# Optimization experiments

Hardware: AMD Instinct MI355X
Metric: run time of the kernel (lower is better)

## Reference

```python
import jax, jax.numpy as jnp
import numpy as np

B, S, D, H = 2, 2048, 2048, 16
HD = D // H
SCALE = 1.0 / np.sqrt(HD)


def setup_inputs() -> dict:
    key = jax.random.key(0)
    ks = jax.random.split(key, 11)
    xav = np.sqrt(6.0 / (D + D))  # xavier uniform bound for square weights
    def w(k):
        return jax.random.uniform(k, (D, D), jnp.float32, -xav, xav)
    return {
        "query": jax.random.normal(ks[0], (B, S, D), jnp.float32),
        "key": jax.random.normal(ks[1], (B, S, D), jnp.float32),
        "value": jax.random.normal(ks[2], (B, S, D), jnp.float32),
        "Wq": w(ks[3]), "bq": jnp.zeros((D,), jnp.float32),
        "Wk": w(ks[4]), "bk": jnp.zeros((D,), jnp.float32),
        "Wv": w(ks[5]), "bv": jnp.zeros((D,), jnp.float32),
        "Wo": w(ks[6]), "bo": jnp.zeros((D,), jnp.float32),
    }


def reference(query, key, value, Wq, bq, Wk, bk, Wv, bv, Wo, bo):
    # projections (torch Linear: x @ W.T + b)
    q = query @ Wq.T + bq
    k = key @ Wk.T + bk
    v = value @ Wv.T + bv
    # [B, H, S, HD]
    q = q.reshape(B, S, H, HD).transpose(0, 2, 1, 3)
    k = k.reshape(B, S, H, HD).transpose(0, 2, 1, 3)
    v = v.reshape(B, S, H, HD).transpose(0, 2, 1, 3)
    scores = jnp.einsum("bhqd,bhkd->bhqk", q, k) * SCALE
    causal = jnp.triu(jnp.ones((S, S), bool), k=1)
    scores = jnp.where(causal, -jnp.inf, scores)
    attn = jax.nn.softmax(scores, axis=-1)  # dropout p=0.0 -> identity
    out = jnp.einsum("bhqk,bhkd->bhqd", attn, v)
    out = out.transpose(0, 2, 1, 3).reshape(B, S, D)
    return out @ Wo.T + bo
```

## Files before the change

### kernel.cpp

```cpp
#include <hip/hip_runtime.h>
#include <hip/hip_bf16.h>


#define LOG2E 1.44269504088896340736f

typedef __attribute__((ext_vector_type(8))) short short8;
typedef __attribute__((ext_vector_type(4))) short short4b;
typedef __attribute__((ext_vector_type(4))) float floatx4;

__device__ __forceinline__ short f2bf(float f) {
  unsigned int u = __builtin_bit_cast(unsigned int, f);
  u += 0x7FFFu + ((u >> 16) & 1u);
  return (short)(u >> 16);
}

__device__ __forceinline__ short4b pack4bf(float a, float b, float c, float d) {
  __hip_bfloat162 lo = __float22bfloat162_rn(float2{a, b});
  __hip_bfloat162 hi = __float22bfloat162_rn(float2{c, d});
  short4b r;
  r[0] = __builtin_bit_cast(short, lo.x); r[1] = __builtin_bit_cast(short, lo.y);
  r[2] = __builtin_bit_cast(short, hi.x); r[3] = __builtin_bit_cast(short, hi.y);
  return r;
}

__device__ __forceinline__ void gl_lds16(const void* g, void* l) {
  __builtin_amdgcn_global_load_lds(
      (const __attribute__((address_space(1))) unsigned int*)g,
      (__attribute__((address_space(3))) unsigned int*)l, 16, 0, 0);
}

__global__ __launch_bounds__(256) void cvt7_k(
    const float* __restrict__ s0, const float* __restrict__ s1,
    const float* __restrict__ s2, const float* __restrict__ s3,
    const float* __restrict__ s4, const float* __restrict__ s5,
    const float* __restrict__ s6,
    unsigned short* __restrict__ d0, unsigned short* __restrict__ d1,
    unsigned short* __restrict__ d2, unsigned short* __restrict__ d3,
    unsigned short* __restrict__ d4, unsigned short* __restrict__ d5,
    unsigned short* __restrict__ d6, int nAct, int nW)
{
  const float* s; unsigned short* d; int n, iters;
  switch (blockIdx.y) {
    case 0: s = s0; d = d0; n = nAct; iters = 4; break;
    case 1: s = s1; d = d1; n = nAct; iters = 4; break;
    case 2: s = s2; d = d2; n = nAct; iters = 4; break;
    case 3: s = s3; d = d3; n = nW;   iters = 1; break;
    case 4: s = s4; d = d4; n = nW;   iters = 1; break;
    case 5: s = s5; d = d5; n = nW;   iters = 1; break;
    default: s = s6; d = d6; n = nW;  iters = 1; break;
  }
#pragma unroll 1
  for (int c = 0; c < iters; ++c) {
    const long i = ((long)(blockIdx.x + c * 2048) * 256 + threadIdx.x) * 8;
    if (i < n) {
      float4 a = *(const float4*)(s + i);
      float4 b = *(const float4*)(s + i + 4);
      short8 v = (short8){f2bf(a.x), f2bf(a.y), f2bf(a.z), f2bf(a.w),
                          f2bf(b.x), f2bf(b.y), f2bf(b.z), f2bf(b.w)};
      *(short8*)(d + i) = v;
    }
  }
}

template<bool OUT_BF16, bool VT_OUT>
__global__ __launch_bounds__(512, 1) void gemm8_k(
    const unsigned short* __restrict__ A, const unsigned short* __restrict__ Bt,
    const float* __restrict__ bias, void* __restrict__ Cptr,
    int M, int N, int K, float alpha)
{
  __shared__ __align__(16) unsigned short As[3][256 * 64];
  __shared__ __align__(16) unsigned short Bs[3][128 * 64];
  (void)M;

  const int tid  = threadIdx.x;
  const int lane = tid & 63;
  const int wave = tid >> 6;
  const int quad = lane >> 4;
  const int l16  = lane & 15;
  const int lx7  = l16 & 7;
  const int wm   = wave >> 1, wn = wave & 1;

  int bx, by;
  if (gridDim.x == 16 && gridDim.y == 16) {
    const int lin  = (int)(blockIdx.y * 16 + blockIdx.x);
    const int xcd  = lin & 7;
    const int slot = lin >> 3;
    bx = (xcd & 1) * 8 + (slot & 7);
    by = (xcd >> 1) * 4 + (slot >> 3);
  } else { bx = (int)blockIdx.x; by = (int)blockIdx.y; }
  const long bm  = (long)by * 256;
  const long bn  = (long)bx * 128;

  const unsigned short* gA[4]; int lAo[4];
  const unsigned short* gB[2]; int lBo[2];
#pragma unroll
  for (int j = 0; j < 4; ++j) {
    const int pa = ((j >> 1) * 16 + wave * 2 + (j & 1)) * 64 + lane;
    const int r = pa >> 3, cp = pa & 7, cs = cp ^ (r & 7);
    gA[j]  = A + (bm + r) * (long)K + cs * 8;
    lAo[j] = pa * 8;
  }
#pragma unroll
  for (int j = 0; j < 2; ++j) {
    const int pb = (wave * 2 + j) * 64 + lane;
    const int r = pb >> 3, cp = pb & 7, cs = cp ^ (r & 7);
    gB[j]  = Bt + (bn + r) * (long)K + cs * 8;
    lBo[j] = pb * 8;
  }

  floatx4 acc[4][4];
#pragma unroll
  for (int i = 0; i < 4; ++i)
#pragma unroll
    for (int j = 0; j < 4; ++j) acc[i][j] = (floatx4){0.f, 0.f, 0.f, 0.f};

  const int NT = K >> 6;

#pragma unroll
  for (int j = 0; j < 4; ++j) gl_lds16(gA[j], &As[0][lAo[j]]);
#pragma unroll
  for (int j = 0; j < 2; ++j) gl_lds16(gB[j], &Bs[0][lBo[j]]);
  if (NT > 1) {
#pragma unroll
    for (int j = 0; j < 4; ++j) gl_lds16(gA[j] + 64, &As[1][lAo[j]]);
#pragma unroll
    for (int j = 0; j < 2; ++j) gl_lds16(gB[j] + 64, &Bs[1][lBo[j]]);
    asm volatile("s_waitcnt vmcnt(6)" ::: "memory");
  } else {
    asm volatile("s_waitcnt vmcnt(0)" ::: "memory");
  }
  __builtin_amdgcn_s_barrier();

  int cur3 = 0;
  for (int t = 0; t < NT; ++t) {
    int nx2 = cur3 + 2; if (nx2 >= 3) nx2 -= 3;
    const long kk2 = (long)(t + 2) * 64;
    const bool st2 = (t + 2) < NT;
    const bool st1 = (t + 1) < NT;
    const unsigned short* Ab = As[cur3];
    const unsigned short* Bb = Bs[cur3];

    if (st2) {
      gl_lds16(gA[0] + kk2, &As[nx2][lAo[0]]);
      gl_lds16(gA[1] + kk2, &As[nx2][lAo[1]]);
      gl_lds16(gA[2] + kk2, &As[nx2][lAo[2]]);
      gl_lds16(gA[3] + kk2, &As[nx2][lAo[3]]);
      gl_lds16(gB[0] + kk2, &Bs[nx2][lBo[0]]);
      gl_lds16(gB[1] + kk2, &Bs[nx2][lBo[1]]);
    }

    short8 af[4][2], bf[4][2];
#pragma unroll
    for (int mt = 0; mt < 4; ++mt)
#pragma unroll
      for (int ks = 0; ks < 2; ++ks)
        af[mt][ks] = *(const short8*)&Ab[(wm * 64 + mt * 16 + l16) * 64 +
                                         (((ks * 4 + quad) ^ lx7) * 8)];
#pragma unroll
    for (int nt = 0; nt < 4; ++nt)
#pragma unroll
      for (int ks = 0; ks < 2; ++ks)
        bf[nt][ks] = *(const short8*)&Bb[(wn * 64 + nt * 16 + l16) * 64 +
                                         (((ks * 4 + quad) ^ lx7) * 8)];

    __builtin_amdgcn_s_setprio(1);
#pragma unroll
    for (int nt = 0; nt < 4; ++nt)
#pragma unroll
      for (int mt = 0; mt < 4; ++mt) {
        acc[mt][nt] = __builtin_amdgcn_mfma_f32_16x16x32_bf16(af[mt][0], bf[nt][0], acc[mt][nt], 0, 0, 0);
        acc[mt][nt] = __builtin_amdgcn_mfma_f32_16x16x32_bf16(af[mt][1], bf[nt][1], acc[mt][nt], 0, 0, 0);
      }
    __builtin_amdgcn_s_setprio(0);

    if (st1) {
      if (st2) asm volatile("s_waitcnt vmcnt(6)" ::: "memory");
      else     asm volatile("s_waitcnt vmcnt(0)" ::: "memory");
    }
    __builtin_amdgcn_s_barrier();

    cur3 = cur3 + 1 >= 3 ? 0 : cur3 + 1;
  }

  if (VT_OUT) {
    __syncthreads();
    unsigned short* Ct = &As[0][0];
#pragma unroll
    for (int nt = 0; nt < 4; ++nt) {
      const int col_l = wn * 64 + nt * 16 + l16;
      const float bval = bias[bn + col_l];
#pragma unroll
      for (int mt = 0; mt < 4; ++mt) {
        const int row_l = wm * 64 + mt * 16 + quad * 4;
#pragma unroll
        for (int rg = 0; rg < 4; ++rg)
          Ct[col_l * 264 + row_l + rg] = (unsigned short)f2bf((acc[mt][nt][rg] + bval) * alpha);
      }
    }
    __syncthreads();
    const int b  = (int)(bm >> 11);
    const int s0 = (int)(bm & 2047);
    const int d   = tid >> 2;
    const int seg = tid & 3;
    unsigned short* dst = (unsigned short*)Cptr +
        ((long)(b * 16 + bx) * 128 + d) * 2048 + s0 + seg * 64;
    const unsigned short* src = &Ct[d * 264 + seg * 64];
#pragma unroll
    for (int c = 0; c < 8; ++c)
      *(uint4*)(dst + c * 8) = *(const uint4*)(src + c * 8);
  } else {
#pragma unroll
    for (int nt = 0; nt < 4; ++nt) {
      const long col = bn + wn * 64 + nt * 16 + l16;
      const float bval = bias[col];
#pragma unroll
      for (int mt = 0; mt < 4; ++mt) {
#pragma unroll
        for (int rg = 0; rg < 4; ++rg) {
          const long row = bm + wm * 64 + mt * 16 + quad * 4 + rg;
          const float v = (acc[mt][nt][rg] + bval) * alpha;
          if (OUT_BF16) ((unsigned short*)Cptr)[row * (long)N + col] = (unsigned short)f2bf(v);
          else          ((float*)Cptr)[row * (long)N + col] = v;
        }
      }
    }
  }
}

template<bool A_BF16, bool OUT_BF16, bool VT_OUT>
__global__ __launch_bounds__(256, 2) void gemm_bias_k(
    const void* __restrict__ Aptr, const float* __restrict__ Bt,
    const float* __restrict__ bias, void* __restrict__ Cptr,
    int M, int N, int K, float alpha)
{
  __shared__ __align__(16) unsigned short smem[128 * 136];
  unsigned short* As = smem;
  unsigned short* Bs = smem + 128 * 40;

  const int tid  = threadIdx.x;
  const int lane = tid & 63;
  const int wave = tid >> 6;
  const int quad = lane >> 4;
  const int l16  = lane & 15;
  const int wr   = wave >> 1, wc = wave & 1;
  const long bm  = (long)blockIdx.y * 128;
  const long bn  = (long)blockIdx.x * 128;

  floatx4 acc[4][4];
#pragma unroll
  for (int i = 0; i < 4; ++i)
#pragma unroll
    for (int j = 0; j < 4; ++j) acc[i][j] = (floatx4){0.f, 0.f, 0.f, 0.f};

  const int srow = tid >> 2;
  const int cc   = tid & 3;

  for (int k0 = 0; k0 < K; k0 += 32) {
    __syncthreads();
#pragma unroll
    for (int r = 0; r < 2; ++r) {
      const int row = srow + r * 64;
      short8 av, bv;
      if (A_BF16) {
        av = *(const short8*)((const unsigned short*)Aptr + (bm + row) * (long)K + k0 + cc * 8);
      } else {
        const float* ap = (const float*)Aptr + (bm + row) * (long)K + k0 + cc * 8;
        float4 f0 = *(const float4*)ap;
        float4 f1 = *(const float4*)(ap + 4);
        av = (short8){f2bf(f0.x), f2bf(f0.y), f2bf(f0.z), f2bf(f0.w),
                      f2bf(f1.x), f2bf(f1.y), f2bf(f1.z), f2bf(f1.w)};
      }
      {
        const float* bp = Bt + (bn + row) * (long)K + k0 + cc * 8;
        float4 g0 = *(const float4*)bp;
        float4 g1 = *(const float4*)(bp + 4);
        bv = (short8){f2bf(g0.x), f2bf(g0.y), f2bf(g0.z), f2bf(g0.w),
                      f2bf(g1.x), f2bf(g1.y), f2bf(g1.z), f2bf(g1.w)};
      }
      *(short8*)&As[row * 40 + cc * 8] = av;
      *(short8*)&Bs[row * 40 + cc * 8] = bv;
    }
    __syncthreads();

    short8 af[4], bf[4];
#pragma unroll
    for (int t = 0; t < 4; ++t) {
      af[t] = *(const short8*)&As[(wr * 64 + t * 16 + l16) * 40 + quad * 8];
      bf[t] = *(const short8*)&Bs[(wc * 64 + t * 16 + l16) * 40 + quad * 8];
    }
#pragma unroll
    for (int mt = 0; mt < 4; ++mt)
#pragma unroll
      for (int nt = 0; nt < 4; ++nt)
        acc[mt][nt] = __builtin_amdgcn_mfma_f32_16x16x32_bf16(af[mt], bf[nt], acc[mt][nt], 0, 0, 0);
  }

  if (VT_OUT) {
    __syncthreads();
    unsigned short* Ct = smem;
#pragma unroll
    for (int nt = 0; nt < 4; ++nt) {
      const long col = bn + wc * 64 + nt * 16 + l16;
      const float bval = bias[col];
      const int col_l = wc * 64 + nt * 16 + l16;
#pragma unroll
      for (int mt = 0; mt < 4; ++mt) {
        const int row_l = wr * 64 + mt * 16 + quad * 4;
#pragma unroll
        for (int rg = 0; rg < 4; ++rg)
          Ct[col_l * 136 + row_l + rg] = (unsigned short)f2bf((acc[mt][nt][rg] + bval) * alpha);
      }
    }
    __syncthreads();
    const int b  = (int)(bm >> 11);
    const int s0 = (int)(bm & 2047);
    const int r    = tid >> 1;
    const int half = tid & 1;
    unsigned short* dst = (unsigned short*)Cptr +
        ((long)(b * 16 + blockIdx.x) * 128 + r) * 2048 + s0 + half * 64;
    const unsigned short* src = &Ct[r * 136 + half * 64];
#pragma unroll
    for (int c = 0; c < 8; ++c)
      *(uint4*)(dst + c * 8) = *(const uint4*)(src + c * 8);
  } else {
#pragma unroll
    for (int nt = 0; nt < 4; ++nt) {
      const long col = bn + wc * 64 + nt * 16 + l16;
      const float bval = bias[col];
#pragma unroll
      for (int mt = 0; mt < 4; ++mt) {
#pragma unroll
        for (int rg = 0; rg < 4; ++rg) {
          const long row = bm + wr * 64 + mt * 16 + quad * 4 + rg;
          const float v = (acc[mt][nt][rg] + bval) * alpha;
          if (OUT_BF16) ((unsigned short*)Cptr)[row * (long)N + col] = (unsigned short)f2bf(v);
          else          ((float*)Cptr)[row * (long)N + col] = v;
        }
      }
    }
  }
}

__global__ __launch_bounds__(256, 2) void flash_attn_k(
    const unsigned short* __restrict__ Q,
    const unsigned short* __restrict__ Kp,
    const unsigned short* __restrict__ Vt,
    unsigned short* __restrict__ O)
{
  constexpr int S = 2048, D = 2048, HD = 128;
  constexpr int PS = 72;

  __shared__ __align__(16) unsigned short Ks[2][64 * 128];
  __shared__ __align__(16) unsigned short Vst[2][128 * 64];
  __shared__ __align__(16) unsigned short Ps[64 * PS];

  const int tid  = threadIdx.x;
  const int lane = tid & 63;
  const int w    = tid >> 6;
  const int quad = lane >> 4;
  const int l16  = lane & 15;
  const int lx7  = l16 & 7;

  const int bx  = blockIdx.x;
  const int by  = blockIdx.y;
  const int idx = by * 2 + (bx >> 3);
  const int bh  = (bx & 7) * 4 + (idx >> 4);
  const int qsel = idx & 15;

  const long headoff = (long)(bh >> 4) * S * D + (long)(bh & 15) * HD;
  const long vtoff   = (long)bh * HD * S;

  const unsigned short* gK[4]; int oK[4];
  const unsigned short* gV[4]; int oV[4];
#pragma unroll
  for (int i = 0; i < 4; ++i) {
    const int p = (w * 4 + i) * 64 + lane;
    { const int r = p >> 4, cp = p & 15, c = cp ^ (r & 7);
      gK[i] = Kp + headoff + (long)r * D + c * 8;  oK[i] = p * 8; }
    { const int r = p >> 3, cp = p & 7, c = cp ^ (r & 7);
      gV[i] = Vt + vtoff + (long)r * S + c * 8;    oV[i] = p * 8; }
  }

#pragma unroll 1
  for (int half = 0; half < 2; ++half) {
    const int qt = half ? (31 - qsel) : qsel;
    const int qbase = qt * 64;
    const int qrow  = qbase + w * 16 + l16;
    const int qloc  = w * 16 + l16;

    short8 aq[4];
    {
      const unsigned short* qp = Q + headoff + (long)qrow * D;
#pragma unroll
      for (int ks = 0; ks < 4; ++ks)
        aq[ks] = *(const short8*)(qp + ks * 32 + quad * 8);
    }

    floatx4 o_acc[8];
#pragma unroll
    for (int t = 0; t < 8; ++t) o_acc[t] = (floatx4){0.f, 0.f, 0.f, 0.f};
    float m_i = -INFINITY;
    float l_p = 0.f;

#pragma unroll
    for (int i = 0; i < 4; ++i) gl_lds16(gK[i], &Ks[0][oK[i]]);
#pragma unroll
    for (int i = 0; i < 4; ++i) gl_lds16(gV[i], &Vst[0][oV[i]]);

    for (int kt = 0; kt <= qt; ++kt) {
      const int cur = kt & 1;
      const int kbase = kt * 64;
      if (kt < qt) {
        const long kb = (long)(kt + 1) * 64;
        const int nb = cur ^ 1;
#pragma unroll
        for (int i = 0; i < 4; ++i) gl_lds16(gK[i] + kb * D, &Ks[nb][oK[i]]);
#pragma unroll
        for (int i = 0; i < 4; ++i) gl_lds16(gV[i] + kb, &Vst[nb][oV[i]]);
        asm volatile("s_waitcnt vmcnt(8)" ::: "memory");
      } else {
        asm volatile("s_waitcnt vmcnt(0)" ::: "memory");
      }
      __builtin_amdgcn_s_barrier();

      const unsigned short* Kb = &Ks[cur][0];
      const unsigned short* Vb = &Vst[cur][0];

      floatx4 sc[4];
#pragma unroll
      for (int nt = 0; nt < 4; ++nt) sc[nt] = (floatx4){0.f, 0.f, 0.f, 0.f};
      __builtin_amdgcn_s_setprio(1);
#pragma unroll
      for (int nt = 0; nt < 4; ++nt) {
        const int krow = nt * 16 + l16;
#pragma unroll
        for (int ks = 0; ks < 4; ++ks) {
          const int cp = (ks * 4 + quad) ^ lx7;
          short8 kf = *(const short8*)&Kb[krow * 128 + cp * 8];
          sc[nt] = __builtin_amdgcn_mfma_f32_16x16x32_bf16(kf, aq[ks], sc[nt], 0, 0, 0);
        }
      }
      __builtin_amdgcn_s_setprio(0);

      float sv[4][4];
      float lmax = -INFINITY;
      if (kt == qt) {
        const int kg0 = kbase + quad * 4;
#pragma unroll
        for (int nt = 0; nt < 4; ++nt)
#pragma unroll
          for (int rg = 0; rg < 4; ++rg) {
            float v = sc[nt][rg];
            if (kg0 + nt * 16 + rg > qrow) v = -INFINITY;
            sv[nt][rg] = v;
            lmax = fmaxf(lmax, v);
          }
      } else {
#pragma unroll
        for (int nt = 0; nt < 4; ++nt)
#pragma unroll
          for (int rg = 0; rg < 4; ++rg) {
            sv[nt][rg] = sc[nt][rg];
            lmax = fmaxf(lmax, sc[nt][rg]);
          }
      }

      float al = 1.0f;
      if (__any(lmax > m_i + 8.0f)) {
        float rmax = fmaxf(lmax, __shfl_xor(lmax, 16));
        rmax = fmaxf(rmax, __shfl_xor(rmax, 32));
        const float mn = fmaxf(m_i, rmax);
        al = exp2f(m_i - mn);
        m_i = mn;
#pragma unroll
        for (int t = 0; t < 8; ++t)
#pragma unroll
          for (int rg = 0; rg < 4; ++rg) o_acc[t][rg] *= al;
      }

      float rsum = 0.f;
#pragma unroll
      for (int nt = 0; nt < 4; ++nt) {
        float p0 = exp2f(sv[nt][0] - m_i), p1 = exp2f(sv[nt][1] - m_i);
        float p2 = exp2f(sv[nt][2] - m_i), p3 = exp2f(sv[nt][3] - m_i);
        rsum += (p0 + p1) + (p2 + p3);
        *(short4b*)&Ps[qloc * PS + nt * 16 + quad * 4] = pack4bf(p0, p1, p2, p3);
      }
      l_p = l_p * al + rsum;

      short8 pf[2];
#pragma unroll
      for (int ks = 0; ks < 2; ++ks)
        pf[ks] = *(const short8*)&Ps[qloc * PS + ks * 32 + quad * 8];

      __builtin_amdgcn_s_setprio(1);
#pragma unroll
      for (int t = 0; t < 8; ++t) {
        const int drow = t * 16 + l16;
#pragma unroll
        for (int ks = 0; ks < 2; ++ks) {
          const int cp = (ks * 4 + quad) ^ lx7;
          short8 vf = *(const short8*)&Vb[drow * 64 + cp * 8];
          o_acc[t] = __builtin_amdgcn_mfma_f32_16x16x32_bf16(vf, pf[ks], o_acc[t], 0, 0, 0);
        }
      }
      __builtin_amdgcn_s_setprio(0);
      __builtin_amdgcn_s_barrier();
    }

    float l_i = l_p + __shfl_xor(l_p, 16);
    l_i += __shfl_xor(l_i, 32);
    const float rl = 1.0f / l_i;
    unsigned short* op = O + headoff + (long)qrow * D;
#pragma unroll
    for (int t = 0; t < 8; ++t) {
      *(short4b*)(op + t * 16 + quad * 4) =
          pack4bf(o_acc[t][0] * rl, o_acc[t][1] * rl, o_acc[t][2] * rl, o_acc[t][3] * rl);
    }
  }
}

extern "C" void kernel_launch(void* const* d_in, const int* in_sizes, int n_in,
                              void* d_out, int out_size, void* d_ws, size_t ws_size,
                              hipStream_t stream) {
  const float* query = (const float*)d_in[0];
  const float* key_  = (const float*)d_in[1];
  const float* value = (const float*)d_in[2];
  const float* Wq = (const float*)d_in[3];
  const float* bq = (const float*)d_in[4];
  const float* Wk = (const float*)d_in[5];
  const float* bk = (const float*)d_in[6];
  const float* Wv = (const float*)d_in[7];
  const float* bv = (const float*)d_in[8];
  const float* Wo = (const float*)d_in[9];
  const float* bo = (const float*)d_in[10];
  float* out = (float*)d_out;

  constexpr int Bz = 2, S = 2048, D = 2048;
  constexpr int M = Bz * S;
  constexpr long NELEM = (long)M * D;
  constexpr long WELEM = (long)D * D;

  const float qscale = 0.08838834764831845f * LOG2E;
  dim3 gridG(D / 128, M / 128);
  dim3 gridG8(D / 128, M / 256);

  const size_t need_full = (size_t)(6 * NELEM + 4 * WELEM) * 2;

  if (ws_size >= need_full) {
    unsigned short* Qp  = (unsigned short*)d_ws;
    unsigned short* Kp  = Qp + NELEM;
    unsigned short* Vt  = Kp + NELEM;
    unsigned short* Xq  = Vt + NELEM;
    unsigned short* Xk  = Xq + NELEM;
    unsigned short* Xv  = Xk + NELEM;
    unsigned short* Wqb = Xv + NELEM;
    unsigned short* Wkb = Wqb + WELEM;
    unsigned short* Wvb = Wkb + WELEM;
    unsigned short* Wob = Wvb + WELEM;
    unsigned short* Oa  = Xq;

    cvt7_k<<<dim3(2048, 7), 256, 0, stream>>>(
        query, key_, value, Wq, Wk, Wv, Wo,
        Xq, Xk, Xv, Wqb, Wkb, Wvb, Wob, (int)NELEM, (int)WELEM);

    gemm8_k<true, false><<<gridG8, 512, 0, stream>>>(Xq, Wqb, bq, Qp, M, D, D, qscale);
    gemm8_k<true, false><<<gridG8, 512, 0, stream>>>(Xk, Wkb, bk, Kp, M, D, D, 1.0f);
    gemm8_k<true, true ><<<gridG8, 512, 0, stream>>>(Xv, Wvb, bv, Vt, M, D, D, 1.0f);

    flash_attn_k<<<dim3(16, 32), 256, 0, stream>>>(Qp, Kp, Vt, Oa);

    gemm8_k<false, false><<<gridG8, 512, 0, stream>>>(Oa, Wob, bo, out, M, D, D, 1.0f);
  } else {
    unsigned short* Qp = (unsigned short*)d_ws;
    unsigned short* Kp = Qp + NELEM;
    unsigned short* Vt = Kp + NELEM;
    unsigned short* Oa = Vt + NELEM;

    gemm_bias_k<false, true, false><<<gridG, 256, 0, stream>>>(query, Wq, bq, Qp, M, D, D, qscale);
    gemm_bias_k<false, true, false><<<gridG, 256, 0, stream>>>(key_,  Wk, bk, Kp, M, D, D, 1.0f);
    gemm_bias_k<false, true, true ><<<gridG, 256, 0, stream>>>(value, Wv, bv, Vt, M, D, D, 1.0f);

    flash_attn_k<<<dim3(16, 32), 256, 0, stream>>>(Qp, Kp, Vt, Oa);

    gemm_bias_k<true, false, false><<<gridG, 256, 0, stream>>>(Oa, Wo, bo, out, M, D, D, 1.0f);
  }
}
```

Baseline: 450.0 us.

## Fuse QKV projections into one launch and split GEMM k-loop into interleaved halves

The three Q/K/V projection GEMMs now run as a single launch, with blockIdx.z selecting the weights, bias and output layout, which removes two launch gaps and their tail effects. The GEMM inner loop is restructured into two half-K phases. Each phase loads its own LDS fragments, issues part of the next tile's global-to-LDS prefetch, and synchronises with extra barriers and lgkmcnt waits before its MFMAs. This spreads the memory traffic across the compute and halves the fragment register footprint, but adds more barriers per iteration. The output projection moves to a specialised fp32-output kernel with compile-time K and N.

```diff
diff --git a/kernel.cpp b/kernel.cpp
--- a/kernel.cpp
+++ b/kernel.cpp
@@ -62,15 +62,119 @@
   }
 }
 
-template<bool OUT_BF16, bool VT_OUT>
-__global__ __launch_bounds__(512, 1) void gemm8_k(
-    const unsigned short* __restrict__ A, const unsigned short* __restrict__ Bt,
-    const float* __restrict__ bias, void* __restrict__ Cptr,
-    int M, int N, int K, float alpha)
+#define GEMM_CORE(A_, Bt_)                                                     \
+  const unsigned short* gA[4]; int lAo[4];                                     \
+  const unsigned short* gB[2]; int lBo[2];                                     \
+  _Pragma("unroll")                                                            \
+  for (int j = 0; j < 4; ++j) {                                                \
+    const int pa = ((j >> 1) * 16 + wave * 2 + (j & 1)) * 64 + lane;           \
+    const int r = pa >> 3, cp = pa & 7, cs = cp ^ (r & 7);                     \
+    gA[j]  = A_ + (bm + r) * (long)K + cs * 8;                                 \
+    lAo[j] = pa * 8;                                                           \
+  }                                                                            \
+  _Pragma("unroll")                                                            \
+  for (int j = 0; j < 2; ++j) {                                                \
+    const int pb = (wave * 2 + j) * 64 + lane;                                 \
+    const int r = pb >> 3, cp = pb & 7, cs = cp ^ (r & 7);                     \
+    gB[j]  = Bt_ + (bn + r) * (long)K + cs * 8;                                \
+    lBo[j] = pb * 8;                                                           \
+  }                                                                            \
+  floatx4 acc[4][4];                                                           \
+  _Pragma("unroll")                                                            \
+  for (int i = 0; i < 4; ++i)                                                  \
+    _Pragma("unroll")                                                          \
+    for (int j = 0; j < 4; ++j) acc[i][j] = (floatx4){0.f, 0.f, 0.f, 0.f};     \
+  const int NT = K >> 6;                                                       \
+  _Pragma("unroll")                                                            \
+  for (int j = 0; j < 4; ++j) gl_lds16(gA[j], &As[0][lAo[j]]);                 \
+  _Pragma("unroll")                                                            \
+  for (int j = 0; j < 2; ++j) gl_lds16(gB[j], &Bs[0][lBo[j]]);                 \
+  if (NT > 1) {                                                                \
+    _Pragma("unroll")                                                          \
+    for (int j = 0; j < 4; ++j) gl_lds16(gA[j] + 64, &As[1][lAo[j]]);          \
+    _Pragma("unroll")                                                          \
+    for (int j = 0; j < 2; ++j) gl_lds16(gB[j] + 64, &Bs[1][lBo[j]]);          \
+    asm volatile("s_waitcnt vmcnt(6)" ::: "memory");                           \
+  } else {                                                                     \
+    asm volatile("s_waitcnt vmcnt(0)" ::: "memory");                           \
+  }                                                                            \
+  __builtin_amdgcn_s_barrier();                                                \
+  int cur3 = 0;                                                                \
+  for (int t = 0; t < NT; ++t) {                                               \
+    int nx2 = cur3 + 2; if (nx2 >= 3) nx2 -= 3;                                \
+    const long kk2 = (long)(t + 2) * 64;                                       \
+    const bool st2 = (t + 2) < NT;                                             \
+    const bool st1 = (t + 1) < NT;                                             \
+    const unsigned short* Ab = As[cur3];                                       \
+    const unsigned short* Bb = Bs[cur3];                                       \
+                                                 \
+    short8 af0[4], bf0[4];                                                     \
+    _Pragma("unroll")                                                          \
+    for (int mt = 0; mt < 4; ++mt)                                             \
+      af0[mt] = *(const short8*)&Ab[(wm * 64 + mt * 16 + l16) * 64 +           \
+                                    ((quad ^ lx7) * 8)];                       \
+    _Pragma("unroll")                                                          \
+    for (int nt = 0; nt < 4; ++nt)                                             \
+      bf0[nt] = *(const short8*)&Bb[(wn * 64 + nt * 16 + l16) * 64 +           \
+                                    ((quad ^ lx7) * 8)];                       \
+    if (st2) { gl_lds16(gA[0] + kk2, &As[nx2][lAo[0]]);                        \
+               gl_lds16(gA[1] + kk2, &As[nx2][lAo[1]]);                        \
+               gl_lds16(gA[2] + kk2, &As[nx2][lAo[2]]); }                      \
+    __builtin_amdgcn_s_barrier();                                              \
+    asm volatile("s_waitcnt lgkmcnt(0)");                                      \
+    __builtin_amdgcn_s_setprio(1);                                             \
+    _Pragma("unroll")                                                          \
+    for (int nt = 0; nt < 4; ++nt)                                             \
+      _Pragma("unroll")                                                        \
+      for (int mt = 0; mt < 4; ++mt)                                           \
+        acc[mt][nt] = __builtin_amdgcn_mfma_f32_16x16x32_bf16(                 \
+            af0[mt], bf0[nt], acc[mt][nt], 0, 0, 0);                           \
+    __builtin_amdgcn_s_setprio(0);                                             \
+    __builtin_amdgcn_s_barrier();                                              \
+                                                 \
+    short8 af1[4], bf1[4];                                                     \
+    _Pragma("unroll")                                                          \
+    for (int mt = 0; mt < 4; ++mt)                                             \
+      af1[mt] = *(const short8*)&Ab[(wm * 64 + mt * 16 + l16) * 64 +           \
+                                    (((4 + quad) ^ lx7) * 8)];                 \
+    _Pragma("unroll")                                                          \
+    for (int nt = 0; nt < 4; ++nt)                                             \
+      bf1[nt] = *(const short8*)&Bb[(wn * 64 + nt * 16 + l16) * 64 +           \
+                                    (((4 + quad) ^ lx7) * 8)];                 \
+    if (st2) { gl_lds16(gA[3] + kk2, &As[nx2][lAo[3]]);                        \
+               gl_lds16(gB[0] + kk2, &Bs[nx2][lBo[0]]);                        \
+               gl_lds16(gB[1] + kk2, &Bs[nx2][lBo[1]]); }                      \
+    __builtin_amdgcn_s_barrier();                                              \
+    asm volatile("s_waitcnt lgkmcnt(0)");                                      \
+    __builtin_amdgcn_s_setprio(1);                                             \
+    _Pragma("unroll")                                                          \
+    for (int nt = 0; nt < 4; ++nt)                                             \
+      _Pragma("unroll")                                                        \
+      for (int mt = 0; mt < 4; ++mt)                                           \
+        acc[mt][nt] = __builtin_amdgcn_mfma_f32_16x16x32_bf16(                 \
+            af1[mt], bf1[nt], acc[mt][nt], 0, 0, 0);                           \
+    __builtin_amdgcn_s_setprio(0);                                             \
+    if (st1) {                                                                 \
+      if (st2) asm volatile("s_waitcnt vmcnt(6)" ::: "memory");                \
+      else     asm volatile("s_waitcnt vmcnt(0)" ::: "memory");                \
+    }                                                                          \
+    __builtin_amdgcn_s_barrier();                                              \
+    cur3 = cur3 + 1 >= 3 ? 0 : cur3 + 1;                                       \
+  }
+
+__global__ __launch_bounds__(512, 1) void gemmqkv_k(
+    const unsigned short* __restrict__ Aq, const unsigned short* __restrict__ Ak,
+    const unsigned short* __restrict__ Av,
+    const unsigned short* __restrict__ Bq, const unsigned short* __restrict__ Bk,
+    const unsigned short* __restrict__ Bv,
+    const float* __restrict__ biq, const float* __restrict__ bik,
+    const float* __restrict__ biv,
+    unsigned short* __restrict__ Cq, unsigned short* __restrict__ Ck,
+    unsigned short* __restrict__ Cv, float qalpha)
 {
+  constexpr int K = 2048, N = 2048;
   __shared__ __align__(16) unsigned short As[3][256 * 64];
   __shared__ __align__(16) unsigned short Bs[3][128 * 64];
-  (void)M;
 
   const int tid  = threadIdx.x;
   const int lane = tid & 63;
@@ -80,109 +184,23 @@
   const int lx7  = l16 & 7;
   const int wm   = wave >> 1, wn = wave & 1;
 
-  int bx, by;
-  if (gridDim.x == 16 && gridDim.y == 16) {
-    const int lin  = (int)(blockIdx.y * 16 + blockIdx.x);
-    const int xcd  = lin & 7;
-    const int slot = lin >> 3;
-    bx = (xcd & 1) * 8 + (slot & 7);
-    by = (xcd >> 1) * 4 + (slot >> 3);
-  } else { bx = (int)blockIdx.x; by = (int)blockIdx.y; }
-  const long bm  = (long)by * 256;
-  const long bn  = (long)bx * 128;
-
-  const unsigned short* gA[4]; int lAo[4];
-  const unsigned short* gB[2]; int lBo[2];
-#pragma unroll
-  for (int j = 0; j < 4; ++j) {
-    const int pa = ((j >> 1) * 16 + wave * 2 + (j & 1)) * 64 + lane;
-    const int r = pa >> 3, cp = pa & 7, cs = cp ^ (r & 7);
-    gA[j]  = A + (bm + r) * (long)K + cs * 8;
-    lAo[j] = pa * 8;
-  }
-#pragma unroll
-  for (int j = 0; j < 2; ++j) {
-    const int pb = (wave * 2 + j) * 64 + lane;
-    const int r = pb >> 3, cp = pb & 7, cs = cp ^ (r & 7);
-    gB[j]  = Bt + (bn + r) * (long)K + cs * 8;
-    lBo[j] = pb * 8;
-  }
-
-  floatx4 acc[4][4];
-#pragma unroll
-  for (int i = 0; i < 4; ++i)
-#pragma unroll
-    for (int j = 0; j < 4; ++j) acc[i][j] = (floatx4){0.f, 0.f, 0.f, 0.f};
-
-  const int NT = K >> 6;
-
-#pragma unroll
-  for (int j = 0; j < 4; ++j) gl_lds16(gA[j], &As[0][lAo[j]]);
-#pragma unroll
-  for (int j = 0; j < 2; ++j) gl_lds16(gB[j], &Bs[0][lBo[j]]);
-  if (NT > 1) {
-#pragma unroll
-    for (int j = 0; j < 4; ++j) gl_lds16(gA[j] + 64, &As[1][lAo[j]]);
-#pragma unroll
-    for (int j = 0; j < 2; ++j) gl_lds16(gB[j] + 64, &Bs[1][lBo[j]]);
-    asm volatile("s_waitcnt vmcnt(6)" ::: "memory");
-  } else {
-    asm volatile("s_waitcnt vmcnt(0)" ::: "memory");
-  }
-  __builtin_amdgcn_s_barrier();
-
-  int cur3 = 0;
-  for (int t = 0; t < NT; ++t) {
-    int nx2 = cur3 + 2; if (nx2 >= 3) nx2 -= 3;
-    const long kk2 = (long)(t + 2) * 64;
-    const bool st2 = (t + 2) < NT;
-    const bool st1 = (t + 1) < NT;
-    const unsigned short* Ab = As[cur3];
-    const unsigned short* Bb = Bs[cur3];
-
-    if (st2) {
-      gl_lds16(gA[0] + kk2, &As[nx2][lAo[0]]);
-      gl_lds16(gA[1] + kk2, &As[nx2][lAo[1]]);
-      gl_lds16(gA[2] + kk2, &As[nx2][lAo[2]]);
-      gl_lds16(gA[3] + kk2, &As[nx2][lAo[3]]);
-      gl_lds16(gB[0] + kk2, &Bs[nx2][lBo[0]]);
-      gl_lds16(gB[1] + kk2, &Bs[nx2][lBo[1]]);
-    }
-
-    short8 af[4][2], bf[4][2];
-#pragma unroll
-    for (int mt = 0; mt < 4; ++mt)
-#pragma unroll
-      for (int ks = 0; ks < 2; ++ks)
-        af[mt][ks] = *(const short8*)&Ab[(wm * 64 + mt * 16 + l16) * 64 +
-                                         (((ks * 4 + quad) ^ lx7) * 8)];
-#pragma unroll
-    for (int nt = 0; nt < 4; ++nt)
-#pragma unroll
-      for (int ks = 0; ks < 2; ++ks)
-        bf[nt][ks] = *(const short8*)&Bb[(wn * 64 + nt * 16 + l16) * 64 +
-                                         (((ks * 4 + quad) ^ lx7) * 8)];
-
-    __builtin_amdgcn_s_setprio(1);
-#pragma unroll
-    for (int nt = 0; nt < 4; ++nt)
-#pragma unroll
-      for (int mt = 0; mt < 4; ++mt) {
-        acc[mt][nt] = __builtin_amdgcn_mfma_f32_16x16x32_bf16(af[mt][0], bf[nt][0], acc[mt][nt], 0, 0, 0);
-        acc[mt][nt] = __builtin_amdgcn_mfma_f32_16x16x32_bf16(af[mt][1], bf[nt][1], acc[mt][nt], 0, 0, 0);
-      }
-    __builtin_amdgcn_s_setprio(0);
-
-    if (st1) {
-      if (st2) asm volatile("s_waitcnt vmcnt(6)" ::: "memory");
-      else     asm volatile("s_waitcnt vmcnt(0)" ::: "memory");
-    }
-    __builtin_amdgcn_s_barrier();
-
-    cur3 = cur3 + 1 >= 3 ? 0 : cur3 + 1;
-  }
-
-  if (VT_OUT) {
+  const unsigned short* A; const unsigned short* Bt; const float* bias;
+  unsigned short* C; float alpha = 1.0f; bool vt = false;
+  if (blockIdx.z == 0)      { A = Aq; Bt = Bq; bias = biq; C = Cq; alpha = qalpha; }
+  else if (blockIdx.z == 1) { A = Ak; Bt = Bk; bias = bik; C = Ck; }
+  else                      { A = Av; Bt = Bv; bias = biv; C = Cv; vt = true; }
+
+  const int lin  = (int)(blockIdx.y * 16 + blockIdx.x);
+  const int xcd  = lin & 7;
+  const int slot = lin >> 3;
+  const int bx = (xcd & 1) * 8 + (slot & 7);
+  const int by = (xcd >> 1) * 4 + (slot >> 3);
+  const long bm = (long)by * 256;
+  const long bn = (long)bx * 128;
+
+  GEMM_CORE(A, Bt)
+
+  if (vt) {
     __syncthreads();
     unsigned short* Ct = &As[0][0];
 #pragma unroll
@@ -202,7 +220,7 @@
     const int s0 = (int)(bm & 2047);
     const int d   = tid >> 2;
     const int seg = tid & 3;
-    unsigned short* dst = (unsigned short*)Cptr +
+    unsigned short* dst = C +
         ((long)(b * 16 + bx) * 128 + d) * 2048 + s0 + seg * 64;
     const unsigned short* src = &Ct[d * 264 + seg * 64];
 #pragma unroll
@@ -218,10 +236,49 @@
 #pragma unroll
         for (int rg = 0; rg < 4; ++rg) {
           const long row = bm + wm * 64 + mt * 16 + quad * 4 + rg;
-          const float v = (acc[mt][nt][rg] + bval) * alpha;
-          if (OUT_BF16) ((unsigned short*)Cptr)[row * (long)N + col] = (unsigned short)f2bf(v);
-          else          ((float*)Cptr)[row * (long)N + col] = v;
+          C[row * (long)N + col] = (unsigned short)f2bf((acc[mt][nt][rg] + bval) * alpha);
         }
+      }
+    }
+  }
+}
+
+__global__ __launch_bounds__(512, 1) void gemmo_k(
+    const unsigned short* __restrict__ A, const unsigned short* __restrict__ Bt,
+    const float* __restrict__ bias, float* __restrict__ C)
+{
+  constexpr int K = 2048, N = 2048;
+  __shared__ __align__(16) unsigned short As[3][256 * 64];
+  __shared__ __align__(16) unsigned short Bs[3][128 * 64];
+
+  const int tid  = threadIdx.x;
+  const int lane = tid & 63;
+  const int wave = tid >> 6;
+  const int quad = lane >> 4;
+  const int l16  = lane & 15;
+  const int lx7  = l16 & 7;
+  const int wm   = wave >> 1, wn = wave & 1;
+
+  const int lin  = (int)(blockIdx.y * 16 + blockIdx.x);
+  const int xcd  = lin & 7;
+  const int slot = lin >> 3;
+  const int bx = (xcd & 1) * 8 + (slot & 7);
+  const int by = (xcd >> 1) * 4 + (slot >> 3);
+  const long bm = (long)by * 256;
+  const long bn = (long)bx * 128;
+
+  GEMM_CORE(A, Bt)
+
+#pragma unroll
+  for (int nt = 0; nt < 4; ++nt) {
+    const long col = bn + wn * 64 + nt * 16 + l16;
+    const float bval = bias[col];
+#pragma unroll
+    for (int mt = 0; mt < 4; ++mt) {
+#pragma unroll
+      for (int rg = 0; rg < 4; ++rg) {
+        const long row = bm + wm * 64 + mt * 16 + quad * 4 + rg;
+        C[row * (long)N + col] = (acc[mt][nt][rg] + bval);
       }
     }
   }
@@ -543,7 +600,6 @@
 
   const float qscale = 0.08838834764831845f * LOG2E;
   dim3 gridG(D / 128, M / 128);
-  dim3 gridG8(D / 128, M / 256);
 
   const size_t need_full = (size_t)(6 * NELEM + 4 * WELEM) * 2;
 
@@ -564,13 +620,12 @@
         query, key_, value, Wq, Wk, Wv, Wo,
         Xq, Xk, Xv, Wqb, Wkb, Wvb, Wob, (int)NELEM, (int)WELEM);
 
-    gemm8_k<true, false><<<gridG8, 512, 0, stream>>>(Xq, Wqb, bq, Qp, M, D, D, qscale);
-    gemm8_k<true, false><<<gridG8, 512, 0, stream>>>(Xk, Wkb, bk, Kp, M, D, D, 1.0f);
-    gemm8_k<true, true ><<<gridG8, 512, 0, stream>>>(Xv, Wvb, bv, Vt, M, D, D, 1.0f);
+    gemmqkv_k<<<dim3(16, 16, 3), 512, 0, stream>>>(
+        Xq, Xk, Xv, Wqb, Wkb, Wvb, bq, bk, bv, Qp, Kp, Vt, qscale);
 
     flash_attn_k<<<dim3(16, 32), 256, 0, stream>>>(Qp, Kp, Vt, Oa);
 
-    gemm8_k<false, false><<<gridG8, 512, 0, stream>>>(Oa, Wob, bo, out, M, D, D, 1.0f);
+    gemmo_k<<<dim3(16, 16), 512, 0, stream>>>(Oa, Wob, bo, out);
   } else {
     unsigned short* Qp = (unsigned short*)d_ws;
     unsigned short* Kp = Qp + NELEM;
```

After: 404.7 us. 10.1% less time.
